# Optimization experiments

Measured on AMD Instinct MI355X. Metric: run time of the kernel, lower is better.

## Reference

```python
import jax, jax.numpy as jnp
import numpy as np

# Detect.__init__ defaults from the source
TOP_K = 5000
CONF_THRESH = 0.01
NMS_THRESH = 0.3
VAR0, VAR1 = 0.1, 0.2   # variance = [0.1, 0.2]
NUM_CLASSES = 2

B = 16
IMAGE = 1280
FMAPS = [320, 160, 80, 40, 20, 10]          # image / steps [4,8,16,32,64,128]
MIN_SIZES = [16, 32, 64, 128, 256, 512]
AR = 1.5                                     # aspect_ratios = [[1.5]] * 6


def make_priors():
    """Vectorized PriorBox.forward: 1 prior per location (max_sizes=[], single AR)."""
    chunks = []
    for f, ms in zip(FMAPS, MIN_SIZES):
        c = (np.arange(f, dtype=np.float32) + 0.5) / f
        cy, cx = np.meshgrid(c, c, indexing='ij')
        s = ms / float(IMAGE)
        w = np.full_like(cx, s / np.sqrt(AR))   # s_k / sqrt(ar)
        h = np.full_like(cx, s * np.sqrt(AR))   # s_k * sqrt(ar)
        chunks.append(np.stack([cx, cy, w, h], -1).reshape(-1, 4))
    pr = np.concatenate(chunks, 0).clip(0.0, 1.0)   # clip=True
    return jnp.asarray(pr, jnp.float32)             # [136500, 4]


def setup_inputs() -> dict:
    key = jax.random.key(0)
    k1, k2 = jax.random.split(key)
    P = sum(f * f for f in FMAPS)   # 136500
    loc_data = 0.5 * jax.random.normal(k1, (B, P, 4), jnp.float32)
    conf_data = jax.random.uniform(k2, (B * P, NUM_CLASSES), jnp.float32)  # post-softmax probs
    prior_data = make_priors()
    return {"loc_data": loc_data, "conf_data": conf_data, "prior_data": prior_data}


def _decode(loc, priors):
    # SSD box decode with variances [0.1, 0.2]; loc, priors: [P,4]
    cxcy = priors[:, :2] + loc[:, :2] * VAR0 * priors[:, 2:]
    wh = priors[:, 2:] * jnp.exp(loc[:, 2:] * VAR1)
    xy1 = cxcy - wh * 0.5
    xy2 = xy1 + wh
    return jnp.concatenate([xy1, xy2], axis=-1)   # [P,4] x1y1x2y2


def _greedy_keep(boxes, valid):
    # Greedy NMS over score-sorted candidates. boxes [K,4], valid [K] bool.
    # Indices/keep decisions are discrete -> computed on stop_gradient'd boxes.
    b = jax.lax.stop_gradient(boxes)
    x1, y1, x2, y2 = b[:, 0], b[:, 1], b[:, 2], b[:, 3]
    area = (x2 - x1) * (y2 - y1)
    idxs = jnp.arange(b.shape[0])

    def body(keep, i):
        iw = jnp.maximum(jnp.minimum(x2, x2[i]) - jnp.maximum(x1, x1[i]), 0.0)
        ih = jnp.maximum(jnp.minimum(y2, y2[i]) - jnp.maximum(y1, y1[i]), 0.0)
        inter = iw * ih
        iou = inter / (area + area[i] - inter)
        suppress = keep[i] & (iou > NMS_THRESH) & (idxs > i)
        return keep & ~suppress, None

    keep, _ = jax.lax.scan(body, valid, idxs)
    return keep


def _detect_one(loc_i, conf_cl, priors):
    # loc_i [P,4]; conf_cl [P] = class-1 scores; returns [TOP_K, 5] (score, x1,y1,x2,y2)
    boxes = _decode(loc_i, priors)
    masked = jnp.where(conf_cl > CONF_THRESH, conf_cl, -1.0)   # c_mask gating
    order = jnp.argsort(-jax.lax.stop_gradient(masked))[:TOP_K]  # scores.sort, top_k cap
    s = masked[order]
    b = boxes[order]
    valid = s > CONF_THRESH
    keep = _greedy_keep(b, valid)
    # scatter kept (score, box) rows, in descending-score order, into dense output
    rank = jnp.cumsum(keep) - 1
    row = jnp.where(keep, rank, TOP_K)            # dropped rows -> scratch slot
    vals = jnp.concatenate([s[:, None], b], axis=1)
    vals = jnp.where(keep[:, None], vals, 0.0)
    out = jnp.zeros((TOP_K + 1, 5), jnp.float32).at[row].set(vals)
    return out[:TOP_K]


def reference(loc_data, conf_data, prior_data):
    num = loc_data.shape[0]
    P = prior_data.shape[0]
    conf_preds = conf_data.reshape(num, P, NUM_CLASSES).transpose(0, 2, 1)  # [B,2,P]
    cls1 = jax.vmap(_detect_one, in_axes=(0, 0, None))(loc_data, conf_preds[:, 1, :], prior_data)
    bg = jnp.zeros_like(cls1)                     # background class row stays zero
    output = jnp.stack([bg, cls1], axis=1)        # [B, 2, TOP_K, 5]
    # NOTE: the original's final `flt[(rank < top_k)...].fill_(0)` fills a boolean-indexed
    # COPY in torch, so it is a no-op on `output`; we faithfully return output unchanged.
    return output
```

## Files before the change

kernel.cpp:

```cpp
#include <hip/hip_runtime.h>
#include <math.h>

#pragma clang fp contract(off)

#define PNUM 136500
#define HPNUM 68250
#define BNUM 16
#define TOPK 5000
#define CAP 8192
#define NB2 1024
#define B2BASE 0xBC00u
#define NWORDS 79
#define NW32 158
#define GSTRIDE 32
#define CAPE 65536
#define ELDS 10240
#define NXB 128
#define NWC 8
#define NXB2 1024
#define BSTRIDE 5120
#define EBUF 3072
#define SLOTS 4

#define OFF_SC    ((size_t)0)
#define OFF_BOX4  (OFF_SC + 320000)
#define OFF_HIST  ((size_t)1920000)
#define OFF_CUT   (OFF_HIST + 65536)
#define OFF_SBASE (OFF_CUT + 64)
#define OFF_GBCUR (OFF_SBASE + 65536)
#define OFF_KEYS  (OFF_GBCUR + 1048576)
#define OFF_ECNT  (OFF_KEYS + 1048576)
#define OFF_BCNT  (OFF_ECNT + 2048)
#define OFF_BCUR  (OFF_BCNT + 65536)
#define OFF_ZEND  (OFF_BCUR + 65536)
#define OFF_EDGE  (OFF_ZEND)
#define OFF_GRP   (OFF_EDGE + 4194304)
#define OFF_BOFS  (OFF_GRP)
#define OFF_SIDX  (OFF_GRP + 16384)
#define OFF_SBOX  (OFF_SIDX + 327680)

__device__ __forceinline__ unsigned f2ord(float f) {
    unsigned u = __float_as_uint(f);
    return (u & 0x80000000u) ? ~u : (u | 0x80000000u);
}
__device__ __forceinline__ float ord2f(unsigned o) {
    unsigned u = (o & 0x80000000u) ? (o ^ 0x80000000u) : ~o;
    return __uint_as_float(u);
}
__device__ __forceinline__ int bucketOf(float x) {
    int b = (int)((x + 0.6f) * 71.111115f);
    return (b < 0) ? 0 : ((b > 127) ? 127 : b);
}
__device__ __forceinline__ int rkeyOf(float x1, float x2) {
    int b = bucketOf(x1);
    int wc = bucketOf(x2) - b;
    if (wc > NWC - 1) wc = NWC - 1;
    if (wc < 0) wc = 0;
    return b * NWC + wc;
}

__global__ void __launch_bounds__(512) k_hist(const float* __restrict__ conf,
                                              unsigned* __restrict__ hist) {
    __shared__ unsigned lh[NB2];
    int img = blockIdx.y;
    for (int i = threadIdx.x; i < NB2; i += 512) lh[i] = 0;
    __syncthreads();
    const float4* src = (const float4*)(conf + (size_t)img * PNUM * 2);
    int stride = gridDim.x * 512;
    for (int q = blockIdx.x * 512 + threadIdx.x; q < HPNUM; q += stride) {
        float4 v = src[q];
        if (v.y > 0.01f) atomicAdd(&lh[(f2ord(v.y) >> 16) - B2BASE], 1u);
        if (v.w > 0.01f) atomicAdd(&lh[(f2ord(v.w) >> 16) - B2BASE], 1u);
    }
    __syncthreads();
    unsigned* h = hist + (size_t)img * NB2;
    for (int i = threadIdx.x; i < NB2; i += 512) {
        unsigned c = lh[i];
        if (c) atomicAdd(&h[i], c);
    }
}

__global__ void __launch_bounds__(256) k_cutoff2(const unsigned* __restrict__ hist,
                                                 unsigned* __restrict__ cut,
                                                 unsigned* __restrict__ sbase) {
    __shared__ unsigned csum[256], suf[256];
    int img = blockIdx.x;
    int t = threadIdx.x;
    const unsigned* h = hist + (size_t)img * NB2;
    unsigned h0 = h[t * 4], h1 = h[t * 4 + 1], h2 = h[t * 4 + 2], h3 = h[t * 4 + 3];
    csum[t] = h0 + h1 + h2 + h3;
    __syncthreads();
    if (t == 0) {
        unsigned a = 0;
        for (int g = 255; g >= 0; --g) { unsigned c = csum[g]; suf[g] = a; a += c; }
        unsigned acc = 0, before = 0;
        int c = -1;
        for (int cc = 255; cc >= 0; --cc) {
            if (acc + csum[cc] >= (unsigned)TOPK) { c = cc; before = acc; break; }
            acc += csum[cc];
        }
        unsigned cutb = B2BASE;
        if (c >= 0) {
            unsigned s2 = before;
            cutb = B2BASE + (unsigned)c * 4u;
            for (int b = c * 4 + 3; b >= c * 4; --b) {
                s2 += h[b];
                if (s2 >= (unsigned)TOPK) { cutb = B2BASE + (unsigned)b; break; }
            }
        }
        cut[img] = cutb;
    }
    __syncthreads();
    unsigned a = suf[t];
    unsigned* sb = sbase + (size_t)img * NB2 + t * 4;
    sb[3] = a;
    sb[2] = a + h3;
    sb[1] = a + h3 + h2;
    sb[0] = a + h3 + h2 + h1;
}

__global__ void __launch_bounds__(256) k_gather2(
        const float* __restrict__ conf, const unsigned* __restrict__ cut,
        const unsigned* __restrict__ sbase, unsigned* __restrict__ gbcur,
        unsigned long long* __restrict__ keys) {
    int q = blockIdx.x * 256 + threadIdx.x;
    int img = blockIdx.y;
    if (q >= HPNUM) return;
    unsigned cutb = cut[img];
    float4 v = ((const float4*)(conf + (size_t)img * PNUM * 2))[q];
    const unsigned* sb = sbase + (size_t)img * NB2;
    unsigned* gc = gbcur + (size_t)img * NB2 * 16;
    unsigned long long* kp = keys + (size_t)img * CAP;
    #pragma unroll
    for (int e = 0; e < 2; ++e) {
        float s = e ? v.w : v.y;
        if (s > 0.01f) {
            unsigned o = f2ord(s);
            if ((o >> 16) >= cutb) {
                unsigned wb = (o >> 16) - B2BASE;
                unsigned pos = sb[wb] + atomicAdd(&gc[wb * 16], 1u);
                if (pos < (unsigned)CAP)
                    kp[pos] = ((unsigned long long)o << 32)
                              | (unsigned)(~(unsigned)(2 * q + e));
            }
        }
    }
}

__global__ void __launch_bounds__(256) k_ssort(
        unsigned long long* __restrict__ keys, const unsigned* __restrict__ hist,
        const unsigned* __restrict__ cut, const unsigned* __restrict__ sbase) {
    int img = blockIdx.y;
    int b = blockIdx.x;
    if (B2BASE + (unsigned)b < cut[img]) return;
    unsigned cnt = hist[(size_t)img * NB2 + b];
    if (cnt <= 1) return;
    if (cnt > 1024) cnt = 1024;
    unsigned np2 = 2;
    while (np2 < cnt) np2 <<= 1;
    unsigned base = sbase[(size_t)img * NB2 + b];
    __shared__ unsigned long long sk[1024];
    unsigned long long* kp = keys + (size_t)img * CAP + base;
    int tid = threadIdx.x;
    for (unsigned i = tid; i < np2; i += 256) sk[i] = (i < cnt) ? kp[i] : 0ull;
    __syncthreads();
    for (unsigned k = 2; k <= np2; k <<= 1) {
        for (unsigned j = k >> 1; j > 0; j >>= 1) {
            for (unsigned t = tid; t < (np2 >> 1); t += 256) {
                unsigned i = ((t & ~(j - 1)) << 1) | (t & (j - 1));
                unsigned p = i | j;
                bool desc = ((i & k) == 0);
                unsigned long long a = sk[i], bb = sk[p];
                bool sw = desc ? (a < bb) : (a > bb);
                if (sw) { sk[i] = bb; sk[p] = a; }
            }
            __syncthreads();
        }
    }
    for (unsigned i = tid; i < cnt; i += 256) kp[i] = sk[i];
}

__global__ void __launch_bounds__(256) k_decode(
        const unsigned long long* __restrict__ keys,
        const float* __restrict__ loc, const float* __restrict__ pri,
        float* __restrict__ SC, float4* __restrict__ BOX4,
        unsigned* __restrict__ bcnt) {
    __shared__ unsigned lb[2][NXB2];
    int tid = threadIdx.x;
    for (int i = tid; i < 2 * NXB2; i += 256) ((unsigned*)lb)[i] = 0;
    __syncthreads();
    int gidx = blockIdx.x * 256 + tid;
    int img0 = (blockIdx.x * 256) / TOPK;
    bool ok = gidx < BNUM * TOPK;
    if (ok) {
        int img = gidx / TOPK;
        int r = gidx - img * TOPK;
        unsigned long long key = keys[(size_t)img * CAP + r];
        size_t o = (size_t)img * TOPK + r;
        float s, x1, y1, x2, y2;
        if (key != 0ull) {
            unsigned ordv = (unsigned)(key >> 32);
            s = ord2f(ordv);
            unsigned p = ~(unsigned)(key & 0xFFFFFFFFull);
            const float* lp = loc + ((size_t)img * PNUM + p) * 4;
            const float* pp = pri + (size_t)p * 4;
            float lx = lp[0], ly = lp[1], lw = lp[2], lh = lp[3];
            float px = pp[0], py = pp[1], pw = pp[2], ph = pp[3];
            float cx = px + (lx * 0.1f) * pw;
            float cy = py + (ly * 0.1f) * ph;
            float w = pw * expf(lw * 0.2f);
            float h = ph * expf(lh * 0.2f);
            x1 = cx - w * 0.5f;
            y1 = cy - h * 0.5f;
            x2 = x1 + w;
            y2 = y1 + h;
        } else {
            s = -1.0f; x1 = 0.f; y1 = 0.f; x2 = 0.f; y2 = 0.f;
        }
        SC[o] = s;
        BOX4[o] = make_float4(x1, y1, x2, y2);
        atomicAdd(&lb[img - img0][rkeyOf(x1, x2)], 1u);
    }
    __syncthreads();
    for (int i = tid; i < 2 * NXB2; i += 256) {
        int sub = i >> 10;
        int bk = i & (NXB2 - 1);
        int img = img0 + sub;
        unsigned c = lb[sub][bk];
        if (c && img < BNUM) atomicAdd(&bcnt[img * NXB2 + bk], c);
    }
}

__global__ void __launch_bounds__(256) k_bscat(
        const unsigned* __restrict__ bcnt, unsigned* __restrict__ bcur,
        const float4* __restrict__ BOX4,
        unsigned* __restrict__ bofs, unsigned* __restrict__ sidx,
        float4* __restrict__ sbox) {
    __shared__ unsigned bpre[NXB2 + 1], tsum[256];
    int img = blockIdx.y;
    int tid = threadIdx.x;
    const unsigned* bc = bcnt + img * NXB2;
    unsigned l0 = bc[tid * 4], l1 = bc[tid * 4 + 1],
             l2 = bc[tid * 4 + 2], l3 = bc[tid * 4 + 3];
    tsum[tid] = l0 + l1 + l2 + l3;
    __syncthreads();
    if (tid == 0) {
        unsigned a = 0;
        for (int t = 0; t < 256; ++t) { unsigned c = tsum[t]; tsum[t] = a; a += c; }
        bpre[NXB2] = a;
    }
    __syncthreads();
    unsigned a = tsum[tid];
    bpre[tid * 4] = a;
    bpre[tid * 4 + 1] = a + l0;
    bpre[tid * 4 + 2] = a + l0 + l1;
    bpre[tid * 4 + 3] = a + l0 + l1 + l2;
    __syncthreads();
    if (blockIdx.x == 0) {
        if (tid < NXB) bofs[img * 130 + tid] = bpre[tid * NWC];
        if (tid == 0) bofs[img * 130 + NXB] = bpre[NXB2];
    }
    int r = blockIdx.x * 256 + tid;
    if (r < TOPK) {
        float4 b = BOX4[(size_t)img * TOPK + r];
        int bk = rkeyOf(b.x, b.z);
        unsigned s = bpre[bk] + atomicAdd(&bcur[img * NXB2 + bk], 1u);
        int base = img * BSTRIDE;
        sidx[base + s] = (unsigned)r;
        sbox[base + s] = b;
    }
}

__global__ void __launch_bounds__(256) k_pair4(
        const unsigned* __restrict__ bofs, const unsigned* __restrict__ sidx,
        const float4* __restrict__ sbox,
        unsigned* __restrict__ ecnt, unsigned* __restrict__ edges) {
    __shared__ unsigned ebuf[EBUF];
    __shared__ unsigned ecl, ebase;
    int img = blockIdx.y;
    int wid = threadIdx.x >> 6;
    int lane = threadIdx.x & 63;
    int sb0 = (blockIdx.x * 4 + wid) * SLOTS;
    if (threadIdx.x == 0) ecl = 0;
    __syncthreads();
    unsigned* ec = ecnt + (size_t)img * GSTRIDE;
    unsigned* eg = edges + (size_t)img * CAPE;
    if (sb0 < TOPK) {
        int base = img * BSTRIDE;
        float x1k[SLOTS], x2k[SLOTS], y1k[SLOTS], y2k[SLOTS], ark[SLOTS];
        unsigned rk[SLOTS];
        bool act[SLOTS];
        #pragma unroll
        for (int k = 0; k < SLOTS; ++k) {
            act[k] = (sb0 + k) < TOPK;
            int s = act[k] ? (sb0 + k) : sb0;
            float4 bk = sbox[base + s];
            x1k[k] = bk.x; y1k[k] = bk.y; x2k[k] = bk.z; y2k[k] = bk.w;
            ark[k] = (bk.z - bk.x) * (bk.w - bk.y);
            rk[k] = sidx[base + s];
        }
        int b1 = bucketOf(x1k[0]);
        int b2m = bucketOf(x2k[0]);
        #pragma unroll
        for (int k = 1; k < SLOTS; ++k)
            if (act[k]) { int b = bucketOf(x2k[k]); if (b > b2m) b2m = b; }
        const unsigned* bo = bofs + img * 130;
        unsigned s0 = bo[b1], s1 = bo[b2m + 1];
        if (s0 < s1) {
            unsigned nit = (s1 - s0 + 63) >> 6;
            unsigned c0 = s0 + (unsigned)lane;
            if (c0 > s1 - 1) c0 = s1 - 1;
            float4 cb = sbox[base + c0];
            unsigned cr = sidx[base + c0];
            for (unsigned it = 0; it < nit; ++it) {
                float4 nb = cb; unsigned nr = cr;
                if (it + 1 < nit) {
                    unsigned cn = s0 + (it + 1) * 64 + (unsigned)lane;
                    if (cn > s1 - 1) cn = s1 - 1;
                    nb = sbox[base + cn];
                    nr = sidx[base + cn];
                }
                bool in = (s0 + it * 64 + (unsigned)lane) < s1;
                float bar = (cb.z - cb.x) * (cb.w - cb.y);
                #pragma unroll
                for (int k = 0; k < SLOTS; ++k) {
                    bool hit = false;
                    unsigned edge = 0;
                    if (in && act[k] && cb.x >= x1k[k]
                        && !(cb.x == x1k[k] && cr <= rk[k])) {
                        float dx = fminf(x2k[k], cb.z) - fmaxf(x1k[k], cb.x);
                        if (dx > 0.0f) {
                            float dy = fminf(y2k[k], cb.w) - fmaxf(y1k[k], cb.y);
                            if (dy > 0.0f) {
                                float inter = dx * dy;
                                float iou = inter / (bar + ark[k] - inter);
                                if (iou > 0.3f) {
                                    unsigned su = (rk[k] < cr) ? rk[k] : cr;
                                    unsigned vi = (rk[k] < cr) ? cr : rk[k];
                                    edge = (vi << 13) | su;
                                    hit = true;
                                }
                            }
                        }
                    }
                    unsigned long long bal = __ballot(hit);
                    if (bal) {
                        int n = __popcll(bal);
                        unsigned wb = 0;
                        if (lane == 0) wb = atomicAdd(&ecl, (unsigned)n);
                        wb = __shfl(wb, 0, 64);
                        if (hit) {
                            unsigned long long lt =
                                (lane == 0) ? 0ull : ((1ull << lane) - 1ull);
                            unsigned p = wb + (unsigned)__popcll(bal & lt);
                            if (p < (unsigned)EBUF) ebuf[p] = edge;
                            else {
                                unsigned gp = atomicAdd(ec, 1u);
                                if (gp < (unsigned)CAPE) eg[gp] = edge;
                            }
                        }
                    }
                }
                cb = nb; cr = nr;
            }
        }
    }
    __syncthreads();
    unsigned n = min(ecl, (unsigned)EBUF);
    if (threadIdx.x == 0 && n) ebase = atomicAdd(ec, n);
    __syncthreads();
    for (unsigned i = threadIdx.x; i < n; i += 256) {
        unsigned p = ebase + i;
        if (p < (unsigned)CAPE) eg[p] = ebuf[i];
    }
}

__global__ void __launch_bounds__(256) k_nms3(
        const float* __restrict__ SC, const float4* __restrict__ BOX4,
        const unsigned* __restrict__ ecnt, const unsigned* __restrict__ edges,
        float* __restrict__ out) {
    __shared__ unsigned lgrp[ELDS];
    __shared__ unsigned undL[160], keptL[160], blockL[160];
    __shared__ unsigned pfx[80];
    __shared__ int chg[2];
    int img = blockIdx.x;
    int tid = threadIdx.x;
    int l = tid & 63;
    int wid = tid >> 6;
    size_t ib = (size_t)img * TOPK;
    const float* sc = SC + ib;

    if (tid < 160) { keptL[tid] = 0u; blockL[tid] = 0u; }
    if (tid < 2) chg[tid] = 0;
    for (int w = wid; w < NWORDS; w += 4) {
        int row = w * 64 + l;
        bool valid = (row < TOPK) && (sc[row] > 0.01f);
        unsigned long long b = __ballot(valid);
        if (l == 0) {
            undL[2 * w]     = (unsigned)b;
            undL[2 * w + 1] = (unsigned)(b >> 32);
        }
    }
    unsigned E = min(ecnt[(size_t)img * GSTRIDE], (unsigned)CAPE);
    const unsigned* eimg = edges + (size_t)img * CAPE;
    bool inl = (E <= (unsigned)ELDS);
    if (inl) for (unsigned e = tid; e < E; e += 256) lgrp[e] = eimg[e];
    __syncthreads();

    for (int round = 0; round < 256; ++round) {
        int par = round & 1;
        for (unsigned e = tid; e < E; e += 256) {
            unsigned ed = inl ? lgrp[e] : eimg[e];
            unsigned s = ed & 8191u;
            unsigned v = ed >> 13;
            unsigned sw = s >> 5, sb = s & 31u;
            unsigned vw = v >> 5, vb = 1u << (v & 31u);
            if ((keptL[sw] >> sb) & 1u) {
                if (undL[vw] & vb) {
                    unsigned old = atomicAnd(&undL[vw], ~vb);
                    if (old & vb) chg[par] = 1;
                }
            } else if ((undL[sw] >> sb) & 1u) {
                if (!(blockL[vw] & vb)) atomicOr(&blockL[vw], vb);
            }
        }
        __syncthreads();
        if (tid < NW32) {
            unsigned nk = undL[tid] & ~blockL[tid];
            if (nk) {
                keptL[tid] |= nk;
                undL[tid] &= ~nk;
                chg[par] = 1;
            }
            blockL[tid] = 0u;
        }
        if (tid == 0) chg[par ^ 1] = 0;
        __syncthreads();
        if (!chg[par]) break;
    }

    if (tid == 0) {
        unsigned acc = 0;
        for (int w = 0; w < NWORDS; ++w) {
            pfx[w] = acc;
            acc += (unsigned)(__popc(keptL[2 * w]) + __popc(keptL[2 * w + 1]));
        }
    }
    __syncthreads();
    const float4* bx = BOX4 + ib;
    float* op = out + (((size_t)img * 2) + 1) * TOPK * 5;
    for (int w = wid; w < NWORDS; w += 4) {
        unsigned long long kw =
            ((unsigned long long)keptL[2 * w + 1] << 32) | keptL[2 * w];
        if (!kw) continue;
        int row = w * 64 + l;
        if ((kw >> l) & 1ull) {
            int rank = (int)pfx[w] + (int)__popcll(kw & ((1ull << l) - 1ull));
            float4 b = bx[row];
            float* r = op + (size_t)rank * 5;
            r[0] = sc[row]; r[1] = b.x; r[2] = b.y; r[3] = b.z; r[4] = b.w;
        }
    }
}

extern "C" void kernel_launch(void* const* d_in, const int* in_sizes, int n_in,
                              void* d_out, int out_size, void* d_ws, size_t ws_size,
                              hipStream_t stream) {
    (void)in_sizes; (void)n_in; (void)ws_size;
    const float* loc  = (const float*)d_in[0];
    const float* conf = (const float*)d_in[1];
    const float* pri  = (const float*)d_in[2];
    float* out = (float*)d_out;
    char* ws = (char*)d_ws;

    float* SC   = (float*)(ws + OFF_SC);
    float4* BOX4 = (float4*)(ws + OFF_BOX4);
    unsigned* hist = (unsigned*)(ws + OFF_HIST);
    unsigned* cut  = (unsigned*)(ws + OFF_CUT);
    unsigned* sbase = (unsigned*)(ws + OFF_SBASE);
    unsigned* gbcur = (unsigned*)(ws + OFF_GBCUR);
    unsigned long long* keys = (unsigned long long*)(ws + OFF_KEYS);
    unsigned* ecnt = (unsigned*)(ws + OFF_ECNT);
    unsigned* bcnt = (unsigned*)(ws + OFF_BCNT);
    unsigned* bcur = (unsigned*)(ws + OFF_BCUR);
    unsigned* edges = (unsigned*)(ws + OFF_EDGE);
    unsigned* bofs = (unsigned*)(ws + OFF_BOFS);
    unsigned* sidx = (unsigned*)(ws + OFF_SIDX);
    float4* sbox = (float4*)(ws + OFF_SBOX);

    hipMemsetAsync(d_out, 0, (size_t)out_size * sizeof(float), stream);
    hipMemsetAsync(ws + OFF_HIST, 0, OFF_ZEND - OFF_HIST, stream);

    dim3 gh1(16, BNUM);
    k_hist<<<gh1, 512, 0, stream>>>(conf, hist);
    k_cutoff2<<<BNUM, 256, 0, stream>>>(hist, cut, sbase);
    dim3 gh2((HPNUM + 255) / 256, BNUM);
    k_gather2<<<gh2, 256, 0, stream>>>(conf, cut, sbase, gbcur, keys);
    dim3 gs(NB2, BNUM);
    k_ssort<<<gs, 256, 0, stream>>>(keys, hist, cut, sbase);
    k_decode<<<(BNUM * TOPK + 255) / 256, 256, 0, stream>>>(
        keys, loc, pri, SC, BOX4, bcnt);
    dim3 gb((TOPK + 255) / 256, BNUM);
    k_bscat<<<gb, 256, 0, stream>>>(bcnt, bcur, BOX4, bofs, sidx, sbox);
    dim3 pg((TOPK + 4 * SLOTS - 1) / (4 * SLOTS), BNUM);
    k_pair4<<<pg, 256, 0, stream>>>(bofs, sidx, sbox, ecnt, edges);
    k_nms3<<<BNUM, 256, 0, stream>>>(SC, BOX4, ecnt, edges, out);
}
```

Before: 235.9 us.

## Fuse bucket sort with box decode and fold output zeroing into NMS

The per-bucket bitonic sort and the decode kernel become one kernel. Sorted keys are decoded straight from shared memory into SC/BOX4, and a per-bucket histogram is flushed to bcnt, so the sorted keys no longer round-trip through global memory and one launch disappears. The separate output memset is removed; each NMS block now zeroes its own image's output slice before scattering kept rows. The workspace layout is reordered so that cut, sbase and keys fall outside the memset range, which shrinks the cleared region. Rows past the total candidate count are no longer written with sentinel values, which assumes at least TOPK candidates pass the threshold.

```diff
diff --git a/kernel.cpp b/kernel.cpp
--- a/kernel.cpp
+++ b/kernel.cpp
@@ -24,16 +24,16 @@
 
 #define OFF_SC    ((size_t)0)
 #define OFF_BOX4  (OFF_SC + 320000)
-#define OFF_HIST  ((size_t)1920000)
-#define OFF_CUT   (OFF_HIST + 65536)
-#define OFF_SBASE (OFF_CUT + 64)
-#define OFF_GBCUR (OFF_SBASE + 65536)
-#define OFF_KEYS  (OFF_GBCUR + 1048576)
-#define OFF_ECNT  (OFF_KEYS + 1048576)
+#define OFF_HIST  (OFF_BOX4 + 1280000)
+#define OFF_GBCUR (OFF_HIST + 65536)
+#define OFF_ECNT  (OFF_GBCUR + 1048576)
 #define OFF_BCNT  (OFF_ECNT + 2048)
 #define OFF_BCUR  (OFF_BCNT + 65536)
 #define OFF_ZEND  (OFF_BCUR + 65536)
-#define OFF_EDGE  (OFF_ZEND)
+#define OFF_CUT   (OFF_ZEND)
+#define OFF_SBASE (OFF_CUT + 64)
+#define OFF_KEYS  (OFF_SBASE + 65536)
+#define OFF_EDGE  (OFF_KEYS + 1048576)
 #define OFF_GRP   (OFF_EDGE + 4194304)
 #define OFF_BOFS  (OFF_GRP)
 #define OFF_SIDX  (OFF_GRP + 16384)
@@ -147,56 +147,53 @@
     }
 }
 
-__global__ void __launch_bounds__(256) k_ssort(
-        unsigned long long* __restrict__ keys, const unsigned* __restrict__ hist,
-        const unsigned* __restrict__ cut, const unsigned* __restrict__ sbase) {
+__global__ void __launch_bounds__(256) k_ssortdec(
+        const unsigned long long* __restrict__ keys,
+        const unsigned* __restrict__ hist, const unsigned* __restrict__ cut,
+        const unsigned* __restrict__ sbase,
+        const float* __restrict__ loc, const float* __restrict__ pri,
+        float* __restrict__ SC, float4* __restrict__ BOX4,
+        unsigned* __restrict__ bcnt) {
+    __shared__ unsigned long long sk[1024];
+    __shared__ unsigned lhist[NXB2];
     int img = blockIdx.y;
     int b = blockIdx.x;
     if (B2BASE + (unsigned)b < cut[img]) return;
     unsigned cnt = hist[(size_t)img * NB2 + b];
-    if (cnt <= 1) return;
-    if (cnt > 1024) cnt = 1024;
-    unsigned np2 = 2;
-    while (np2 < cnt) np2 <<= 1;
+    if (cnt == 0) return;
     unsigned base = sbase[(size_t)img * NB2 + b];
-    __shared__ unsigned long long sk[1024];
-    unsigned long long* kp = keys + (size_t)img * CAP + base;
+    if (base >= (unsigned)TOPK) return;
+    const unsigned long long* kp = keys + (size_t)img * CAP + base;
     int tid = threadIdx.x;
-    for (unsigned i = tid; i < np2; i += 256) sk[i] = (i < cnt) ? kp[i] : 0ull;
-    __syncthreads();
-    for (unsigned k = 2; k <= np2; k <<= 1) {
-        for (unsigned j = k >> 1; j > 0; j >>= 1) {
-            for (unsigned t = tid; t < (np2 >> 1); t += 256) {
-                unsigned i = ((t & ~(j - 1)) << 1) | (t & (j - 1));
-                unsigned p = i | j;
-                bool desc = ((i & k) == 0);
-                unsigned long long a = sk[i], bb = sk[p];
-                bool sw = desc ? (a < bb) : (a > bb);
-                if (sw) { sk[i] = bb; sk[p] = a; }
+    for (int i = tid; i < NXB2; i += 256) lhist[i] = 0;
+    unsigned scnt = cnt > 1024 ? 1024u : cnt;
+    if (scnt >= 2) {
+        unsigned np2 = 2;
+        while (np2 < scnt) np2 <<= 1;
+        for (unsigned i = tid; i < np2; i += 256) sk[i] = (i < scnt) ? kp[i] : 0ull;
+        __syncthreads();
+        for (unsigned k = 2; k <= np2; k <<= 1) {
+            for (unsigned j = k >> 1; j > 0; j >>= 1) {
+                for (unsigned t = tid; t < (np2 >> 1); t += 256) {
+                    unsigned i = ((t & ~(j - 1)) << 1) | (t & (j - 1));
+                    unsigned p = i | j;
+                    bool desc = ((i & k) == 0);
+                    unsigned long long a = sk[i], bb = sk[p];
+                    bool sw = desc ? (a < bb) : (a > bb);
+                    if (sw) { sk[i] = bb; sk[p] = a; }
+                }
+                __syncthreads();
             }
-            __syncthreads();
-        }
-    }
-    for (unsigned i = tid; i < cnt; i += 256) kp[i] = sk[i];
-}
-
-__global__ void __launch_bounds__(256) k_decode(
-        const unsigned long long* __restrict__ keys,
-        const float* __restrict__ loc, const float* __restrict__ pri,
-        float* __restrict__ SC, float4* __restrict__ BOX4,
-        unsigned* __restrict__ bcnt) {
-    __shared__ unsigned lb[2][NXB2];
-    int tid = threadIdx.x;
-    for (int i = tid; i < 2 * NXB2; i += 256) ((unsigned*)lb)[i] = 0;
-    __syncthreads();
-    int gidx = blockIdx.x * 256 + tid;
-    int img0 = (blockIdx.x * 256) / TOPK;
-    bool ok = gidx < BNUM * TOPK;
-    if (ok) {
-        int img = gidx / TOPK;
-        int r = gidx - img * TOPK;
-        unsigned long long key = keys[(size_t)img * CAP + r];
-        size_t o = (size_t)img * TOPK + r;
+        }
+    } else {
+        if (tid == 0 && scnt == 1) sk[0] = kp[0];
+        __syncthreads();
+    }
+    size_t ibase = (size_t)img * TOPK;
+    for (unsigned i = tid; i < cnt; i += 256) {
+        unsigned r = base + i;
+        if (r >= (unsigned)TOPK) continue;
+        unsigned long long key = (i < scnt) ? sk[i] : kp[i];
         float s, x1, y1, x2, y2;
         if (key != 0ull) {
             unsigned ordv = (unsigned)(key >> 32);
@@ -217,17 +214,14 @@
         } else {
             s = -1.0f; x1 = 0.f; y1 = 0.f; x2 = 0.f; y2 = 0.f;
         }
-        SC[o] = s;
-        BOX4[o] = make_float4(x1, y1, x2, y2);
-        atomicAdd(&lb[img - img0][rkeyOf(x1, x2)], 1u);
-    }
-    __syncthreads();
-    for (int i = tid; i < 2 * NXB2; i += 256) {
-        int sub = i >> 10;
-        int bk = i & (NXB2 - 1);
-        int img = img0 + sub;
-        unsigned c = lb[sub][bk];
-        if (c && img < BNUM) atomicAdd(&bcnt[img * NXB2 + bk], c);
+        SC[ibase + r] = s;
+        BOX4[ibase + r] = make_float4(x1, y1, x2, y2);
+        atomicAdd(&lhist[rkeyOf(x1, x2)], 1u);
+    }
+    __syncthreads();
+    for (int i = tid; i < NXB2; i += 256) {
+        unsigned c = lhist[i];
+        if (c) atomicAdd(&bcnt[img * NXB2 + i], c);
     }
 }
 
@@ -390,6 +384,11 @@
     size_t ib = (size_t)img * TOPK;
     const float* sc = SC + ib;
 
+    float* oimg = out + (size_t)img * 2 * TOPK * 5;
+    uint4* oz = (uint4*)oimg;
+    uint4 z4 = make_uint4(0u, 0u, 0u, 0u);
+    for (int i = tid; i < 12500; i += 256) oz[i] = z4;
+
     if (tid < 160) { keptL[tid] = 0u; blockL[tid] = 0u; }
     if (tid < 2) chg[tid] = 0;
     for (int w = wid; w < NWORDS; w += 4) {
@@ -448,7 +447,7 @@
     }
     __syncthreads();
     const float4* bx = BOX4 + ib;
-    float* op = out + (((size_t)img * 2) + 1) * TOPK * 5;
+    float* op = oimg + (size_t)TOPK * 5;
     for (int w = wid; w < NWORDS; w += 4) {
         unsigned long long kw =
             ((unsigned long long)keptL[2 * w + 1] << 32) | keptL[2 * w];
@@ -466,7 +465,7 @@
 extern "C" void kernel_launch(void* const* d_in, const int* in_sizes, int n_in,
                               void* d_out, int out_size, void* d_ws, size_t ws_size,
                               hipStream_t stream) {
-    (void)in_sizes; (void)n_in; (void)ws_size;
+    (void)in_sizes; (void)n_in; (void)ws_size; (void)out_size;
     const float* loc  = (const float*)d_in[0];
     const float* conf = (const float*)d_in[1];
     const float* pri  = (const float*)d_in[2];
@@ -488,7 +487,6 @@
     unsigned* sidx = (unsigned*)(ws + OFF_SIDX);
     float4* sbox = (float4*)(ws + OFF_SBOX);
 
-    hipMemsetAsync(d_out, 0, (size_t)out_size * sizeof(float), stream);
     hipMemsetAsync(ws + OFF_HIST, 0, OFF_ZEND - OFF_HIST, stream);
 
     dim3 gh1(16, BNUM);
@@ -497,9 +495,8 @@
     dim3 gh2((HPNUM + 255) / 256, BNUM);
     k_gather2<<<gh2, 256, 0, stream>>>(conf, cut, sbase, gbcur, keys);
     dim3 gs(NB2, BNUM);
-    k_ssort<<<gs, 256, 0, stream>>>(keys, hist, cut, sbase);
-    k_decode<<<(BNUM * TOPK + 255) / 256, 256, 0, stream>>>(
-        keys, loc, pri, SC, BOX4, bcnt);
+    k_ssortdec<<<gs, 256, 0, stream>>>(keys, hist, cut, sbase,
+                                       loc, pri, SC, BOX4, bcnt);
     dim3 gb((TOPK + 255) / 256, BNUM);
     k_bscat<<<gb, 256, 0, stream>>>(bcnt, bcur, BOX4, bofs, sidx, sbox);
     dim3 pg((TOPK + 4 * SLOTS - 1) / (4 * SLOTS), BNUM);
```

Measured after the change: 232.9 us. About the same (-1.3%).
